# Performance work log

Measured on AMD Instinct MI355X. Metric: run time of the kernel, lower is better.

The kernel has to match this reference:

```python
import jax, jax.numpy as jnp
import numpy as np

B, D, H, T = 4096, 256, 266, 51   # batch, dim, dim+10 hidden, timegrid points
S = T - 1                          # Euler steps
KAPPA, SIGMA = 1.0, 1.0
EPS = 1e-5                         # BatchNorm eps (torch default)


def setup_inputs() -> dict:
    key = jax.random.key(0)
    ks = iter(jax.random.split(key, 16))

    def lin(nin, nout, prefix=()):
        return jax.random.normal(next(ks), prefix + (nin, nout), jnp.float32) / np.float32(np.sqrt(nin))

    inp = {}
    inp["x"] = jax.random.normal(next(ks), (B, D), jnp.float32)
    # per-timestep stacks: Linear+BN params for i_h1, h1_h2, and Linear for h2_o
    inp["W1"] = lin(D, H, (S,));  inp["b1"] = jnp.zeros((S, H));  inp["g1"] = jnp.ones((S, H));  inp["be1"] = jnp.zeros((S, H))
    inp["W2"] = lin(H, H, (S,));  inp["b2"] = jnp.zeros((S, H));  inp["g2"] = jnp.ones((S, H));  inp["be2"] = jnp.zeros((S, H))
    inp["W3"] = lin(H, D, (S,));  inp["b3"] = jnp.zeros((S, D))
    # v0 head: three hiddenLayers (Linear+BN+ReLU), last one width 1
    inp["vW1"] = lin(D, H);  inp["vb1"] = jnp.zeros((H,));  inp["vg1"] = jnp.ones((H,));  inp["vbe1"] = jnp.zeros((H,))
    inp["vW2"] = lin(H, H);  inp["vb2"] = jnp.zeros((H,));  inp["vg2"] = jnp.ones((H,));  inp["vbe2"] = jnp.zeros((H,))
    inp["vW3"] = lin(H, 1);  inp["vb3"] = jnp.zeros((1,));  inp["vg3"] = jnp.ones((1,));  inp["vbe3"] = jnp.zeros((1,))
    # frozen external netAlpha: (dim+1) -> H -> dim MLP
    inp["aW1"] = lin(D + 1, H);  inp["ab1"] = jnp.zeros((H,))
    inp["aW2"] = lin(H, D);      inp["ab2"] = jnp.zeros((D,))
    # law (population mean per step), timegrid, Brownian increments xi
    inp["law"] = jax.random.normal(next(ks), (S, D), jnp.float32) * 0.1
    inp["timegrid"] = jnp.linspace(0.0, 1.0, T, dtype=jnp.float32)
    inp["xi"] = jax.random.normal(next(ks), (S, B, D), jnp.float32)
    return inp


def _bn(h, g, b):
    # BatchNorm1d in training mode: batch stats (biased variance), affine
    mu = h.mean(axis=0)
    var = h.var(axis=0)
    return g * (h - mu) / jnp.sqrt(var + EPS) + b


def _hid(h, W, b, g, be):
    return jax.nn.relu(_bn(h @ W + b, g, be))


def reference(x, W1, b1, g1, be1, W2, b2, g2, be2, W3, b3,
              vW1, vb1, vg1, vbe1, vW2, vb2, vg2, vbe2, vW3, vb3, vg3, vbe3,
              aW1, ab1, aW2, ab2, law, timegrid, xi):
    x0 = x
    # v0 head evaluated on initial x (i == 0 branch)
    v0 = _hid(x0, vW1, vb1, vg1, vbe1)
    v0 = _hid(v0, vW2, vb2, vg2, vbe2)
    v0 = _hid(v0, vW3, vb3, vg3, vbe3)            # [B, 1]

    hs = jnp.diff(timegrid)                        # [S]
    ts = timegrid[:-1]                             # [S]

    def step(carry, inp):
        xc, vc = carry
        (W1i, b1i, g1i, be1i, W2i, b2i, g2i, be2i, W3i, b3i, lawi, ti, hi, xii) = inp
        h1 = _hid(xc, W1i, b1i, g1i, be1i)
        h2 = _hid(h1, W2i, b2i, g2i, be2i)
        grad = h2 @ W3i + b3i                      # [B, D]
        tx = jnp.concatenate([jnp.full((xc.shape[0], 1), ti, xc.dtype), xc], axis=1)
        alpha = jax.nn.relu(tx @ aW1 + ab1) @ aW2 + ab2   # [B, D]
        f = 0.5 * KAPPA * jnp.sum((xc - lawi) ** 2, axis=1) + 0.5 * jnp.sum(alpha ** 2, axis=1)
        sq = SIGMA * jnp.sqrt(hi)
        # diag(grad @ (sigma*sqrt(h)*xi).T) == row-wise dot product
        ito = sq * jnp.sum(grad * xii, axis=1)     # [B]
        vn = vc - (f * hi)[:, None] + ito[:, None]
        xn = xc + alpha * hi + sq * xii
        return (xn, vn), xn

    (xf, v), xs = jax.lax.scan(
        step, (x0, v0),
        (W1, b1, g1, be1, W2, b2, g2, be2, W3, b3, law, ts, hs, xi))
    path = jnp.concatenate([x0[None], xs], axis=0)  # [T, B, D]
    return (v, xf, path)
```

## Files before the change

### kernel.cpp

```cpp
#include <hip/hip_runtime.h>
#include <math.h>

#define B_   4096
#define D_   256
#define H_   266
#define T_   51
#define S_   50
#define HP   320
#define EPSF 1e-5f

typedef __bf16 bf16_t;
typedef __bf16 bf16x8 __attribute__((ext_vector_type(8)));
typedef float  f32x4  __attribute__((ext_vector_type(4)));

#define BM 64
#define BN 64
#define BK 64
#define LDST 72

struct Job {
  const float* A; int lda; int Ka;
  const float* g; const float* be;
  const float* asum; const float* asq;
  int bnA;
  const bf16_t* Wt; int ldw;
  const float* bias;
  const float* trow; const float* tg; int tidx;
  float* C; int ldc; int N; int relu;
  float* ssum; float* ssq;
};

__device__ __forceinline__ void load16(const float* p, float* a) {
  const float4* q = (const float4*)p;
  float4 v0 = q[0], v1 = q[1], v2 = q[2], v3 = q[3];
  a[0]=v0.x; a[1]=v0.y; a[2]=v0.z;  a[3]=v0.w;
  a[4]=v1.x; a[5]=v1.y; a[6]=v1.z;  a[7]=v1.w;
  a[8]=v2.x; a[9]=v2.y; a[10]=v2.z; a[11]=v2.w;
  a[12]=v3.x; a[13]=v3.y; a[14]=v3.z; a[15]=v3.w;
}

__global__ __launch_bounds__(256) void mfma_gemm(Job j0, Job j1, float invB) {
  Job j = blockIdx.z ? j1 : j0;
  __shared__ bf16_t As[BM][LDST];
  __shared__ bf16_t Ws[BN][LDST];
  __shared__ float sc[HP], sh[HP];

  const int tid = threadIdx.x;
  const int r0 = blockIdx.y * BM;
  const int c0 = blockIdx.x * BN;

  if (j.bnA) {
    for (int k = tid; k < HP; k += 256) {
      if (k < j.Ka) {
        float mu  = j.asum[k] * invB;
        float var = j.asq[k] * invB - mu * mu;
        float s   = j.g[k] * rsqrtf(var + EPSF);
        sc[k] = s; sh[k] = j.be[k] - mu * s;
      } else { sc[k] = 0.f; sh[k] = 0.f; }
    }
  }

  const int wave = tid >> 6;
  const int lane = tid & 63;
  const int wr = (wave >> 1) * 32;
  const int wc = (wave & 1) * 32;
  const int l16 = lane & 15;
  const int lk8 = (lane >> 4) * 8;

  f32x4 acc[2][2] = {};

  const int arow = tid >> 2;
  const int kseg = (tid & 3) * 16;

  const int niter = (j.Ka + BK - 1) / BK;

  const float*  Abase = j.A + (size_t)(r0 + arow) * j.lda + kseg;
  const int     crow  = c0 + arow;
  const bf16_t* Wbase = j.Wt + (size_t)crow * j.ldw + kseg;
  const bool    wok   = crow < j.N;

  float a16[16];
  uint4 wv0 = make_uint4(0,0,0,0), wv1 = make_uint4(0,0,0,0);

  load16(Abase, a16);
  if (wok) {
    const uint4* q = (const uint4*)Wbase;
    wv0 = q[0]; wv1 = q[1];
  }

  for (int it = 0; it < niter; ++it) {
    const int kb = it * BK + kseg;

    __syncthreads();

    bf16x8 p0, p1;
    if (j.bnA) {
      #pragma unroll
      for (int i = 0; i < 8; ++i)
        p0[i] = (bf16_t)fmaxf(fmaf(a16[i], sc[kb + i], sh[kb + i]), 0.f);
      #pragma unroll
      for (int i = 0; i < 8; ++i)
        p1[i] = (bf16_t)fmaxf(fmaf(a16[8 + i], sc[kb + 8 + i], sh[kb + 8 + i]), 0.f);
    } else {
      #pragma unroll
      for (int i = 0; i < 8; ++i) {
        float t = (kb + i < j.Ka) ? a16[i] : 0.f;
        p0[i] = (bf16_t)t;
      }
      #pragma unroll
      for (int i = 0; i < 8; ++i) {
        float t = (kb + 8 + i < j.Ka) ? a16[8 + i] : 0.f;
        p1[i] = (bf16_t)t;
      }
    }
    *(bf16x8*)&As[arow][kseg]     = p0;
    *(bf16x8*)&As[arow][kseg + 8] = p1;
    *(uint4*)&Ws[arow][kseg]      = wv0;
    *(uint4*)&Ws[arow][kseg + 8]  = wv1;

    __syncthreads();

    if (it + 1 < niter) {
      load16(Abase + (size_t)(it + 1) * BK, a16);
      if (wok) {
        const uint4* q = (const uint4*)(Wbase + (size_t)(it + 1) * BK);
        wv0 = q[0]; wv1 = q[1];
      }
    }

    bf16x8 af[2][2], bfr[2][2];
    #pragma unroll
    for (int mi = 0; mi < 2; ++mi)
      #pragma unroll
      for (int kk = 0; kk < 2; ++kk)
        af[mi][kk] = *(const bf16x8*)&As[wr + mi*16 + l16][kk*32 + lk8];
    #pragma unroll
    for (int ni = 0; ni < 2; ++ni)
      #pragma unroll
      for (int kk = 0; kk < 2; ++kk)
        bfr[ni][kk] = *(const bf16x8*)&Ws[wc + ni*16 + l16][kk*32 + lk8];
    #pragma unroll
    for (int kk = 0; kk < 2; ++kk)
      #pragma unroll
      for (int mi = 0; mi < 2; ++mi)
        #pragma unroll
        for (int ni = 0; ni < 2; ++ni)
          acc[mi][ni] = __builtin_amdgcn_mfma_f32_16x16x32_bf16(af[mi][kk], bfr[ni][kk], acc[mi][ni], 0, 0, 0);
  }

  float tb = j.trow ? j.tg[j.tidx] : 0.f;
  #pragma unroll
  for (int ni = 0; ni < 2; ++ni) {
    int col = c0 + wc + ni*16 + l16;
    bool cok = col < j.N;
    float bias = cok ? j.bias[col] : 0.f;
    if (j.trow && cok) bias = fmaf(tb, j.trow[col], bias);
    float s = 0.f, q = 0.f;
    #pragma unroll
    for (int mi = 0; mi < 2; ++mi) {
      #pragma unroll
      for (int r = 0; r < 4; ++r) {
        float v = acc[mi][ni][r] + bias;
        if (j.relu) v = fmaxf(v, 0.f);
        int row = r0 + wr + mi*16 + ((lane >> 4) << 2) + r;
        if (cok) j.C[(size_t)row * j.ldc + col] = v;
        s += v; q += v * v;
      }
    }
    if (j.ssum) {
      s += __shfl_xor(s, 16); q += __shfl_xor(q, 16);
      s += __shfl_xor(s, 32); q += __shfl_xor(q, 32);
      if (lane < 16) {
        int col2 = c0 + wc + ni*16 + lane;
        if (col2 < j.N) { atomicAdd(&j.ssum[col2], s); atomicAdd(&j.ssq[col2], q); }
      }
    }
  }
}

__global__ __launch_bounds__(256) void wconv(const float* __restrict__ in, bf16_t* __restrict__ out,
                                             int K, int N, int Kp, int total) {
  for (int idx = blockIdx.x * 256 + threadIdx.x; idx < total; idx += gridDim.x * 256) {
    int k = idx % Kp; int rest = idx / Kp; int n = rest % N; int s = rest / N;
    float v = (k < K) ? in[((size_t)s * K + k) * N + n] : 0.f;
    out[idx] = (bf16_t)v;
  }
}

__global__ __launch_bounds__(256) void matvec_bn(const float* __restrict__ A, int lda,
                                                 const float* __restrict__ g, const float* __restrict__ be,
                                                 const float* __restrict__ asum, const float* __restrict__ asq,
                                                 const float* __restrict__ w, const float* __restrict__ bptr,
                                                 float* __restrict__ y, float* ssum, float* ssq,
                                                 int K, float invB) {
  int r = blockIdx.x;
  float acc = 0.f;
  for (int k = threadIdx.x; k < K; k += 256) {
    float mu  = asum[k] * invB;
    float var = asq[k] * invB - mu * mu;
    float s   = g[k] * rsqrtf(var + EPSF);
    float val = fmaxf(fmaf(A[(size_t)r * lda + k], s, be[k] - mu * s), 0.f);
    acc += val * w[k];
  }
  __shared__ float sred[256];
  sred[threadIdx.x] = acc; __syncthreads();
  for (int st = 128; st > 0; st >>= 1) {
    if (threadIdx.x < st) sred[threadIdx.x] += sred[threadIdx.x + st];
    __syncthreads();
  }
  if (threadIdx.x == 0) {
    float v = sred[0] + bptr[0];
    y[r] = v;
    atomicAdd(ssum, v); atomicAdd(ssq, v * v);
  }
}

__global__ __launch_bounds__(256) void v0_fin(const float* __restrict__ y, float* v,
                                              const float* g, const float* be,
                                              const float* ssum, const float* ssq,
                                              int M, float invM) {
  int r = blockIdx.x * blockDim.x + threadIdx.x;
  if (r < M) {
    float mu  = ssum[0] * invM;
    float var = ssq[0] * invM - mu * mu;
    float t = g[0] * (y[r] - mu) * rsqrtf(var + EPSF) + be[0];
    v[r] = fmaxf(t, 0.f);
  }
}

__global__ __launch_bounds__(256) void update_step(const float* __restrict__ xc,
                                                   float* __restrict__ xn,
                                                   const float* __restrict__ alpha,
                                                   const float* __restrict__ grad,
                                                   const float* __restrict__ xi_i,
                                                   const float* __restrict__ law_i,
                                                   const float* __restrict__ tg, int i,
                                                   float* __restrict__ v) {
  const int lane = threadIdx.x & 63;
  const int wv   = threadIdx.x >> 6;
  const int r    = blockIdx.x * 4 + wv;
  const float hi = tg[i + 1] - tg[i];
  const float sq = sqrtf(hi);
  const size_t off = (size_t)r * D_ + lane * 4;
  float4 x4 = *(const float4*)(xc + off);
  float4 a4 = *(const float4*)(alpha + off);
  float4 g4 = *(const float4*)(grad + off);
  float4 z4 = *(const float4*)(xi_i + off);
  float4 l4 = *(const float4*)(law_i + lane * 4);
  float xv[4] = {x4.x, x4.y, x4.z, x4.w};
  float av[4] = {a4.x, a4.y, a4.z, a4.w};
  float gv[4] = {g4.x, g4.y, g4.z, g4.w};
  float zv[4] = {z4.x, z4.y, z4.z, z4.w};
  float lv[4] = {l4.x, l4.y, l4.z, l4.w};
  float sf = 0.f, si = 0.f;
  float ov[4];
  #pragma unroll
  for (int e = 0; e < 4; ++e) {
    float df = xv[e] - lv[e];
    sf += df * df + av[e] * av[e];
    si += gv[e] * zv[e];
    ov[e] = xv[e] + av[e] * hi + sq * zv[e];
  }
  #pragma unroll
  for (int d = 1; d < 64; d <<= 1) {
    sf += __shfl_xor(sf, d);
    si += __shfl_xor(si, d);
  }
  if (lane == 0) v[r] = v[r] - 0.5f * sf * hi + sq * si;
  float4 o; o.x = ov[0]; o.y = ov[1]; o.z = ov[2]; o.w = ov[3];
  *(float4*)(xn + off) = o;
}

extern "C" void kernel_launch(void* const* d_in, const int* in_sizes, int n_in,
                              void* d_out, int out_size, void* d_ws, size_t ws_size,
                              hipStream_t stream) {
  const float* x    = (const float*)d_in[0];
  const float* W1   = (const float*)d_in[1];
  const float* b1   = (const float*)d_in[2];
  const float* g1   = (const float*)d_in[3];
  const float* be1  = (const float*)d_in[4];
  const float* W2   = (const float*)d_in[5];
  const float* b2   = (const float*)d_in[6];
  const float* g2   = (const float*)d_in[7];
  const float* be2  = (const float*)d_in[8];
  const float* W3   = (const float*)d_in[9];
  const float* b3   = (const float*)d_in[10];
  const float* vW1  = (const float*)d_in[11];
  const float* vb1  = (const float*)d_in[12];
  const float* vg1  = (const float*)d_in[13];
  const float* vbe1 = (const float*)d_in[14];
  const float* vW2  = (const float*)d_in[15];
  const float* vb2  = (const float*)d_in[16];
  const float* vg2  = (const float*)d_in[17];
  const float* vbe2 = (const float*)d_in[18];
  const float* vW3  = (const float*)d_in[19];
  const float* vb3  = (const float*)d_in[20];
  const float* vg3  = (const float*)d_in[21];
  const float* vbe3 = (const float*)d_in[22];
  const float* aW1  = (const float*)d_in[23];
  const float* ab1  = (const float*)d_in[24];
  const float* aW2  = (const float*)d_in[25];
  const float* ab2  = (const float*)d_in[26];
  const float* law  = (const float*)d_in[27];
  const float* tg   = (const float*)d_in[28];
  const float* xi   = (const float*)d_in[29];

  float* out    = (float*)d_out;
  float* v_out  = out;
  float* xf_out = out + B_;
  float* path   = out + B_ + (size_t)B_ * D_;

  float* ws   = (float*)d_ws;
  float* h1   = ws;
  float* h2   = h1 + (size_t)B_ * HP;
  float* ah   = h2 + (size_t)B_ * HP;
  float* grad = ah + (size_t)B_ * HP;
  float* alp  = grad + (size_t)B_ * D_;
  float* yraw = alp + (size_t)B_ * D_;
  float* stats = yraw + B_;
  const int NSLOT = 2 * S_ + 3;

  bf16_t* wbuf = (bf16_t*)(stats + (size_t)NSLOT * 2 * HP);
  bf16_t* W1t  = wbuf;
  bf16_t* W2t  = W1t + (size_t)S_ * H_ * 256;
  bf16_t* W3t  = W2t + (size_t)S_ * H_ * 320;
  bf16_t* aW1t = W3t + (size_t)S_ * 256 * 320;
  bf16_t* aW2t = aW1t + (size_t)H_ * 256;
  bf16_t* vW1t = aW2t + (size_t)256 * 320;
  bf16_t* vW2t = vW1t + (size_t)H_ * 256;

  hipMemsetAsync(stats, 0, (size_t)NSLOT * 2 * HP * sizeof(float), stream);
  hipMemcpyAsync(path, x, (size_t)B_ * D_ * sizeof(float), hipMemcpyDeviceToDevice, stream);

  auto ssum = [&](int s) { return stats + (size_t)s * 2 * HP; };
  auto ssq  = [&](int s) { return stats + (size_t)s * 2 * HP + HP; };

  dim3 blk(256);
  const float invB = 1.0f / (float)B_;
  const int MT   = B_ / BM;
  const int NT_H = (H_ + BN - 1) / BN;
  const int NT_D = D_ / BN;

  wconv<<<dim3(1024), blk, 0, stream>>>(W1,        W1t,  256, H_,  256, S_ * H_ * 256);
  wconv<<<dim3(1024), blk, 0, stream>>>(W2,        W2t,  H_,  H_,  320, S_ * H_ * 320);
  wconv<<<dim3(1024), blk, 0, stream>>>(W3,        W3t,  H_,  256, 320, S_ * 256 * 320);
  wconv<<<dim3(256),  blk, 0, stream>>>(aW1 + H_,  aW1t, 256, H_,  256, H_ * 256);
  wconv<<<dim3(256),  blk, 0, stream>>>(aW2,       aW2t, H_,  256, 320, 256 * 320);
  wconv<<<dim3(256),  blk, 0, stream>>>(vW1,       vW1t, 256, H_,  256, H_ * 256);
  wconv<<<dim3(256),  blk, 0, stream>>>(vW2,       vW2t, H_,  H_,  320, H_ * 320);

  {
    Job jv1 = {x, D_, D_, nullptr, nullptr, nullptr, nullptr, 0,
               vW1t, 256, vb1, nullptr, nullptr, 0,
               h1, HP, H_, 0, ssum(100), ssq(100)};
    mfma_gemm<<<dim3(NT_H, MT, 1), blk, 0, stream>>>(jv1, jv1, invB);
    Job jv2 = {h1, HP, H_, vg1, vbe1, ssum(100), ssq(100), 1,
               vW2t, 320, vb2, nullptr, nullptr, 0,
               h2, HP, H_, 0, ssum(101), ssq(101)};
    mfma_gemm<<<dim3(NT_H, MT, 1), blk, 0, stream>>>(jv2, jv2, invB);
    matvec_bn<<<dim3(B_), blk, 0, stream>>>(h2, HP, vg2, vbe2, ssum(101), ssq(101),
                                            vW3, vb3, yraw, ssum(102), ssq(102), H_, invB);
    v0_fin<<<dim3(16), blk, 0, stream>>>(yraw, v_out, vg3, vbe3, ssum(102), ssq(102), B_, invB);
  }

  for (int i = 0; i < S_; ++i) {
    const float* xc = path + (size_t)i * B_ * D_;
    float* xn       = path + (size_t)(i + 1) * B_ * D_;

    Job ja = {xc, D_, D_, nullptr, nullptr, nullptr, nullptr, 0,
              W1t + (size_t)i * H_ * 256, 256, b1 + (size_t)i * H_, nullptr, nullptr, 0,
              h1, HP, H_, 0, ssum(2 * i), ssq(2 * i)};
    Job jb = {xc, D_, D_, nullptr, nullptr, nullptr, nullptr, 0,
              aW1t, 256, ab1, aW1, tg, i,
              ah, HP, H_, 1, nullptr, nullptr};
    mfma_gemm<<<dim3(NT_H, MT, 2), blk, 0, stream>>>(ja, jb, invB);

    Job jc = {h1, HP, H_, g1 + (size_t)i * H_, be1 + (size_t)i * H_, ssum(2 * i), ssq(2 * i), 1,
              W2t + (size_t)i * H_ * 320, 320, b2 + (size_t)i * H_, nullptr, nullptr, 0,
              h2, HP, H_, 0, ssum(2 * i + 1), ssq(2 * i + 1)};
    mfma_gemm<<<dim3(NT_H, MT, 1), blk, 0, stream>>>(jc, jc, invB);

    Job jd = {h2, HP, H_, g2 + (size_t)i * H_, be2 + (size_t)i * H_, ssum(2 * i + 1), ssq(2 * i + 1), 1,
              W3t + (size_t)i * 256 * 320, 320, b3 + (size_t)i * D_, nullptr, nullptr, 0,
              grad, D_, D_, 0, nullptr, nullptr};
    Job je = {ah, HP, H_, nullptr, nullptr, nullptr, nullptr, 0,
              aW2t, 320, ab2, nullptr, nullptr, 0,
              alp, D_, D_, 0, nullptr, nullptr};
    mfma_gemm<<<dim3(NT_D, MT, 2), blk, 0, stream>>>(jd, je, invB);

    update_step<<<dim3(B_ / 4), blk, 0, stream>>>(xc, xn, alp, grad,
                                                  xi + (size_t)i * B_ * D_,
                                                  law + (size_t)i * D_, tg, i, v_out);
  }

  hipMemcpyAsync(xf_out, path + (size_t)S_ * B_ * D_,
                 (size_t)B_ * D_ * sizeof(float), hipMemcpyDeviceToDevice, stream);
}
```

Before: 2.572 ms.

## Fuse Euler update into GEMM epilogues and defer grad GEMM to next step

Removes the separate update_step kernel and the grad/alpha intermediate buffers. The alpha GEMM epilogue now writes x_{n+1} and accumulates the drift term of v by atomics. The grad GEMM for step i is deferred and launched in the same grid as step i+1's first GEMMs, with its Ito term folded into the epilogue, and a final vadd adds the accumulated v. This cuts kernel launches and global round trips and improves GPU fill by sharing grids. In exchange it adds many per-row atomics, uncoalesced scalar loads in the epilogue, and extra early-exit blocks in grids sized for the larger N.

```diff
diff --git a/kernel.cpp b/kernel.cpp
--- a/kernel.cpp
+++ b/kernel.cpp
@@ -28,6 +28,9 @@
   const float* trow; const float* tg; int tidx;
   float* C; int ldc; int N; int relu;
   float* ssum; float* ssq;
+  int mode;
+  const float* xc; const float* xi; const float* law;
+  float* xn; float* vacc;
 };
 
 __device__ __forceinline__ void load16(const float* p, float* a) {
@@ -39,15 +42,18 @@
   a[12]=v3.x; a[13]=v3.y; a[14]=v3.z; a[15]=v3.w;
 }
 
-__global__ __launch_bounds__(256) void mfma_gemm(Job j0, Job j1, float invB) {
-  Job j = blockIdx.z ? j1 : j0;
+__global__ __launch_bounds__(256) void mfma_gemm(Job j0, Job j1, Job j2, float invB) {
+  Job j = (blockIdx.z == 0) ? j0 : ((blockIdx.z == 1) ? j1 : j2);
+
+  const int r0 = blockIdx.y * BM;
+  const int c0 = blockIdx.x * BN;
+  if (c0 >= j.N) return;
+
   __shared__ bf16_t As[BM][LDST];
   __shared__ bf16_t Ws[BN][LDST];
   __shared__ float sc[HP], sh[HP];
 
   const int tid = threadIdx.x;
-  const int r0 = blockIdx.y * BM;
-  const int c0 = blockIdx.x * BN;
 
   if (j.bnA) {
     for (int k = tid; k < HP; k += 256) {
@@ -149,30 +155,76 @@
   }
 
   float tb = j.trow ? j.tg[j.tidx] : 0.f;
+  float vv[2][2][4];
   #pragma unroll
   for (int ni = 0; ni < 2; ++ni) {
     int col = c0 + wc + ni*16 + l16;
     bool cok = col < j.N;
     float bias = cok ? j.bias[col] : 0.f;
     if (j.trow && cok) bias = fmaf(tb, j.trow[col], bias);
-    float s = 0.f, q = 0.f;
-    #pragma unroll
-    for (int mi = 0; mi < 2; ++mi) {
+    #pragma unroll
+    for (int mi = 0; mi < 2; ++mi)
       #pragma unroll
       for (int r = 0; r < 4; ++r) {
         float v = acc[mi][ni][r] + bias;
         if (j.relu) v = fmaxf(v, 0.f);
+        vv[mi][ni][r] = v;
+      }
+  }
+
+  if (j.mode == 0) {
+    #pragma unroll
+    for (int ni = 0; ni < 2; ++ni) {
+      int col = c0 + wc + ni*16 + l16;
+      bool cok = col < j.N;
+      float s = 0.f, q = 0.f;
+      #pragma unroll
+      for (int mi = 0; mi < 2; ++mi)
+        #pragma unroll
+        for (int r = 0; r < 4; ++r) {
+          float v = vv[mi][ni][r];
+          int row = r0 + wr + mi*16 + ((lane >> 4) << 2) + r;
+          if (cok) j.C[(size_t)row * j.ldc + col] = v;
+          s += v; q += v * v;
+        }
+      if (j.ssum) {
+        s += __shfl_xor(s, 16); q += __shfl_xor(q, 16);
+        s += __shfl_xor(s, 32); q += __shfl_xor(q, 32);
+        if (lane < 16) {
+          int col2 = c0 + wc + ni*16 + lane;
+          if (col2 < j.N) { atomicAdd(&j.ssum[col2], s); atomicAdd(&j.ssq[col2], q); }
+        }
+      }
+    }
+  } else {
+    float hi = j.tg[j.tidx + 1] - j.tg[j.tidx];
+    float sq = sqrtf(hi);
+    #pragma unroll
+    for (int mi = 0; mi < 2; ++mi) {
+      #pragma unroll
+      for (int r = 0; r < 4; ++r) {
         int row = r0 + wr + mi*16 + ((lane >> 4) << 2) + r;
-        if (cok) j.C[(size_t)row * j.ldc + col] = v;
-        s += v; q += v * v;
-      }
-    }
-    if (j.ssum) {
-      s += __shfl_xor(s, 16); q += __shfl_xor(q, 16);
-      s += __shfl_xor(s, 32); q += __shfl_xor(q, 32);
-      if (lane < 16) {
-        int col2 = c0 + wc + ni*16 + lane;
-        if (col2 < j.N) { atomicAdd(&j.ssum[col2], s); atomicAdd(&j.ssq[col2], q); }
+        float part = 0.f;
+        #pragma unroll
+        for (int ni = 0; ni < 2; ++ni) {
+          int col = c0 + wc + ni*16 + l16;
+          size_t off = (size_t)row * D_ + col;
+          float v = vv[mi][ni][r];
+          if (j.mode == 1) {
+            float xcv = j.xc[off];
+            float xiv = j.xi[off];
+            float lw  = j.law[col];
+            j.xn[off] = xcv + v * hi + sq * xiv;
+            float df = xcv - lw;
+            part += df * df + v * v;
+          } else {
+            part += v * j.xi[off];
+          }
+        }
+        part += __shfl_xor(part, 1); part += __shfl_xor(part, 2);
+        part += __shfl_xor(part, 4); part += __shfl_xor(part, 8);
+        if (l16 == 0)
+          atomicAdd(&j.vacc[row], (j.mode == 1) ? -0.5f * hi * part : sq * part);
       }
     }
   }
@@ -228,47 +280,9 @@
   }
 }
 
-__global__ __launch_bounds__(256) void update_step(const float* __restrict__ xc,
-                                                   float* __restrict__ xn,
-                                                   const float* __restrict__ alpha,
-                                                   const float* __restrict__ grad,
-                                                   const float* __restrict__ xi_i,
-                                                   const float* __restrict__ law_i,
-                                                   const float* __restrict__ tg, int i,
-                                                   float* __restrict__ v) {
-  const int lane = threadIdx.x & 63;
-  const int wv   = threadIdx.x >> 6;
-  const int r    = blockIdx.x * 4 + wv;
-  const float hi = tg[i + 1] - tg[i];
-  const float sq = sqrtf(hi);
-  const size_t off = (size_t)r * D_ + lane * 4;
-  float4 x4 = *(const float4*)(xc + off);
-  float4 a4 = *(const float4*)(alpha + off);
-  float4 g4 = *(const float4*)(grad + off);
-  float4 z4 = *(const float4*)(xi_i + off);
-  float4 l4 = *(const float4*)(law_i + lane * 4);
-  float xv[4] = {x4.x, x4.y, x4.z, x4.w};
-  float av[4] = {a4.x, a4.y, a4.z, a4.w};
-  float gv[4] = {g4.x, g4.y, g4.z, g4.w};
-  float zv[4] = {z4.x, z4.y, z4.z, z4.w};
-  float lv[4] = {l4.x, l4.y, l4.z, l4.w};
-  float sf = 0.f, si = 0.f;
-  float ov[4];
-  #pragma unroll
-  for (int e = 0; e < 4; ++e) {
-    float df = xv[e] - lv[e];
-    sf += df * df + av[e] * av[e];
-    si += gv[e] * zv[e];
-    ov[e] = xv[e] + av[e] * hi + sq * zv[e];
-  }
-  #pragma unroll
-  for (int d = 1; d < 64; d <<= 1) {
-    sf += __shfl_xor(sf, d);
-    si += __shfl_xor(si, d);
-  }
-  if (lane == 0) v[r] = v[r] - 0.5f * sf * hi + sq * si;
-  float4 o; o.x = ov[0]; o.y = ov[1]; o.z = ov[2]; o.w = ov[3];
-  *(float4*)(xn + off) = o;
+__global__ __launch_bounds__(256) void vadd(float* __restrict__ v, const float* __restrict__ vacc, int M) {
+  int r = blockIdx.x * 256 + threadIdx.x;
+  if (r < M) v[r] += vacc[r];
 }
 
 extern "C" void kernel_launch(void* const* d_in, const int* in_sizes, int n_in,
@@ -314,13 +328,12 @@
   float* h1   = ws;
   float* h2   = h1 + (size_t)B_ * HP;
   float* ah   = h2 + (size_t)B_ * HP;
-  float* grad = ah + (size_t)B_ * HP;
-  float* alp  = grad + (size_t)B_ * D_;
-  float* yraw = alp + (size_t)B_ * D_;
+  float* yraw = ah + (size_t)B_ * HP;
   float* stats = yraw + B_;
   const int NSLOT = 2 * S_ + 3;
-
-  bf16_t* wbuf = (bf16_t*)(stats + (size_t)NSLOT * 2 * HP);
+  float* vacc = stats + (size_t)NSLOT * 2 * HP;
+
+  bf16_t* wbuf = (bf16_t*)(vacc + B_);
   bf16_t* W1t  = wbuf;
   bf16_t* W2t  = W1t + (size_t)S_ * H_ * 256;
   bf16_t* W3t  = W2t + (size_t)S_ * H_ * 320;
@@ -329,7 +342,7 @@
   bf16_t* vW1t = aW2t + (size_t)256 * 320;
   bf16_t* vW2t = vW1t + (size_t)H_ * 256;
 
-  hipMemsetAsync(stats, 0, (size_t)NSLOT * 2 * HP * sizeof(float), stream);
+  hipMemsetAsync(stats, 0, ((size_t)NSLOT * 2 * HP + B_) * sizeof(float), stream);
   hipMemcpyAsync(path, x, (size_t)B_ * D_ * sizeof(float), hipMemcpyDeviceToDevice, stream);
 
   auto ssum = [&](int s) { return stats + (size_t)s * 2 * HP; };
@@ -352,46 +365,56 @@
   {
     Job jv1 = {x, D_, D_, nullptr, nullptr, nullptr, nullptr, 0,
                vW1t, 256, vb1, nullptr, nullptr, 0,
-               h1, HP, H_, 0, ssum(100), ssq(100)};
-    mfma_gemm<<<dim3(NT_H, MT, 1), blk, 0, stream>>>(jv1, jv1, invB);
+               h1, HP, H_, 0, ssum(100), ssq(100),
+               0, nullptr, nullptr, nullptr, nullptr, nullptr};
+    mfma_gemm<<<dim3(NT_H, MT, 1), blk, 0, stream>>>(jv1, jv1, jv1, invB);
     Job jv2 = {h1, HP, H_, vg1, vbe1, ssum(100), ssq(100), 1,
                vW2t, 320, vb2, nullptr, nullptr, 0,
-               h2, HP, H_, 0, ssum(101), ssq(101)};
-    mfma_gemm<<<dim3(NT_H, MT, 1), blk, 0, stream>>>(jv2, jv2, invB);
+               h2, HP, H_, 0, ssum(101), ssq(101),
+               0, nullptr, nullptr, nullptr, nullptr, nullptr};
+    mfma_gemm<<<dim3(NT_H, MT, 1), blk, 0, stream>>>(jv2, jv2, jv2, invB);
     matvec_bn<<<dim3(B_), blk, 0, stream>>>(h2, HP, vg2, vbe2, ssum(101), ssq(101),
                                             vW3, vb3, yraw, ssum(102), ssq(102), H_, invB);
     v0_fin<<<dim3(16), blk, 0, stream>>>(yraw, v_out, vg3, vbe3, ssum(102), ssq(102), B_, invB);
   }
 
+  Job jd_prev;
   for (int i = 0; i < S_; ++i) {
-    const float* xc = path + (size_t)i * B_ * D_;
-    float* xn       = path + (size_t)(i + 1) * B_ * D_;
+    const float* xc   = path + (size_t)i * B_ * D_;
+    float* xn         = path + (size_t)(i + 1) * B_ * D_;
+    const float* xi_i = xi + (size_t)i * B_ * D_;
+    const float* lw_i = law + (size_t)i * D_;
 
     Job ja = {xc, D_, D_, nullptr, nullptr, nullptr, nullptr, 0,
               W1t + (size_t)i * H_ * 256, 256, b1 + (size_t)i * H_, nullptr, nullptr, 0,
-              h1, HP, H_, 0, ssum(2 * i), ssq(2 * i)};
+              h1, HP, H_, 0, ssum(2 * i), ssq(2 * i),
+              0, nullptr, nullptr, nullptr, nullptr, nullptr};
     Job jb = {xc, D_, D_, nullptr, nullptr, nullptr, nullptr, 0,
               aW1t, 256, ab1, aW1, tg, i,
-              ah, HP, H_, 1, nullptr, nullptr};
-    mfma_gemm<<<dim3(NT_H, MT, 2), blk, 0, stream>>>(ja, jb, invB);
+              ah, HP, H_, 1, nullptr, nullptr,
+              0, nullptr, nullptr, nullptr, nullptr, nullptr};
+    if (i == 0)
+      mfma_gemm<<<dim3(NT_H, MT, 2), blk, 0, stream>>>(ja, jb, jb, invB);
+    else
+      mfma_gemm<<<dim3(NT_H, MT, 3), blk, 0, stream>>>(ja, jb, jd_prev, invB);
 
     Job jc = {h1, HP, H_, g1 + (size_t)i * H_, be1 + (size_t)i * H_, ssum(2 * i), ssq(2 * i), 1,
               W2t + (size_t)i * H_ * 320, 320, b2 + (size_t)i * H_, nullptr, nullptr, 0,
-              h2, HP, H_, 0, ssum(2 * i + 1), ssq(2 * i + 1)};
-    mfma_gemm<<<dim3(NT_H, MT, 1), blk, 0, stream>>>(jc, jc, invB);
-
-    Job jd = {h2, HP, H_, g2 + (size_t)i * H_, be2 + (size_t)i * H_, ssum(2 * i + 1), ssq(2 * i + 1), 1,
-              W3t + (size_t)i * 256 * 320, 320, b3 + (size_t)i * D_, nullptr, nullptr, 0,
-              grad, D_, D_, 0, nullptr, nullptr};
+              h2, HP, H_, 0, ssum(2 * i + 1), ssq(2 * i + 1),
+              0, nullptr, nullptr, nullptr, nullptr, nullptr};
     Job je = {ah, HP, H_, nullptr, nullptr, nullptr, nullptr, 0,
-              aW2t, 320, ab2, nullptr, nullptr, 0,
-              alp, D_, D_, 0, nullptr, nullptr};
-    mfma_gemm<<<dim3(NT_D, MT, 2), blk, 0, stream>>>(jd, je, invB);
-
-    update_step<<<dim3(B_ / 4), blk, 0, stream>>>(xc, xn, alp, grad,
-                                                  xi + (size_t)i * B_ * D_,
-                                                  law + (size_t)i * D_, tg, i, v_out);
-  }
+              aW2t, 320, ab2, nullptr, tg, i,
+              nullptr, 0, D_, 0, nullptr, nullptr,
+              1, xc, xi_i, lw_i, xn, vacc};
+    mfma_gemm<<<dim3(NT_H, MT, 2), blk, 0, stream>>>(jc, je, je, invB);
+
+    jd_prev = Job{h2, HP, H_, g2 + (size_t)i * H_, be2 + (size_t)i * H_, ssum(2 * i + 1), ssq(2 * i + 1), 1,
+                  W3t + (size_t)i * 256 * 320, 320, b3 + (size_t)i * D_, nullptr, tg, i,
+                  nullptr, 0, D_, 0, nullptr, nullptr,
+                  2, nullptr, xi_i, nullptr, nullptr, vacc};
+  }
+  mfma_gemm<<<dim3(NT_D, MT, 1), blk, 0, stream>>>(jd_prev, jd_prev, jd_prev, invB);
+  vadd<<<dim3(16), blk, 0, stream>>>(v_out, vacc, B_);
 
   hipMemcpyAsync(xf_out, path + (size_t)S_ * B_ * D_,
                  (size_t)B_ * D_ * sizeof(float), hipMemcpyDeviceToDevice, stream);
```

Result: no change. 2.579 ms (+0.3%).
